# Optimization experiments

Measured on AMD Instinct MI355X. Metric: run time of the kernel, lower is better.

The kernel has to match this reference:

```python
import jax, jax.numpy as jnp
import numpy as np

GRID_RES = 256
SCALE = 1.0
N_POINTS = 2_000_000


def setup_inputs() -> dict:
    key = jax.random.key(0)
    k_pos, k_grid = jax.random.split(key)
    # points in [-0.6, 0.6]^3 so a realistic fraction falls inside the grid (|x| < scale/2)
    pos = jax.random.uniform(k_pos, (N_POINTS, 3), dtype=jnp.float32, minval=-0.6, maxval=0.6)
    # learned parameter: dense voxel grid with (r, g, b, density) per cell, init ~ U[0,1) like torch.rand
    voxel_grid = jax.random.uniform(k_grid, (GRID_RES, GRID_RES, GRID_RES, 4), dtype=jnp.float32)
    return {"pos": pos, "voxel_grid": voxel_grid}


def reference(pos, voxel_grid):
    grid_res = voxel_grid.shape[0]
    scale = SCALE
    half = scale / 2
    x, y, z = pos[:, 0], pos[:, 1], pos[:, 2]
    # mask of points inside the voxel grid volume
    cond = (jnp.abs(x) < half) & (jnp.abs(y) < half) & (jnp.abs(z) < half)

    inv_cell = grid_res / scale  # 1 / (scale / grid_res)
    offset = grid_res / 2

    def to_idx(v):
        # torch .type(torch.long) truncates toward zero; values here are in (0, grid_res)
        # so truncation == floor. Out-of-grid points are given a safe dummy index 0.
        i = (v * inv_cell + offset).astype(jnp.int32)
        return jnp.where(cond, i, 0)

    ix, iy, iz = to_idx(x), to_idx(y), to_idx(z)
    gathered = voxel_grid[ix, iy, iz]                      # [N, 4] gather
    cad = jnp.where(cond[:, None], gathered, jnp.zeros((), pos.dtype))  # masked points stay 0
    colors = jax.nn.sigmoid(cad[:, :3])                    # sigmoid(0)=0.5 for masked pts, as in torch
    density = jax.nn.relu(cad[:, 3])
    return colors, density
```

## Files before the change

kernel.cpp:

```cpp
#include <hip/hip_runtime.h>


#define GRID_RES 256

__global__ __launch_bounds__(256) void nerf_voxel_kernel(
    const float* __restrict__ pos,
    const float4* __restrict__ grid,
    float* __restrict__ colors,
    float* __restrict__ density,
    int n)
{
    int i = blockIdx.x * blockDim.x + threadIdx.x;
    if (i >= n) return;

    float x = pos[3 * i + 0];
    float y = pos[3 * i + 1];
    float z = pos[3 * i + 2];

    bool cond = (fabsf(x) < 0.5f) & (fabsf(y) < 0.5f) & (fabsf(z) < 0.5f);

    float4 cad = make_float4(0.0f, 0.0f, 0.0f, 0.0f);
    if (cond) {
        int ix = (int)(__fadd_rn(__fmul_rn(x, 256.0f), 128.0f));
        int iy = (int)(__fadd_rn(__fmul_rn(y, 256.0f), 128.0f));
        int iz = (int)(__fadd_rn(__fmul_rn(z, 256.0f), 128.0f));
        size_t idx = ((size_t)ix * GRID_RES + (size_t)iy) * GRID_RES + (size_t)iz;
        cad = grid[idx];
    }

    float c0 = 1.0f / (1.0f + __expf(-cad.x));
    float c1 = 1.0f / (1.0f + __expf(-cad.y));
    float c2 = 1.0f / (1.0f + __expf(-cad.z));
    float d  = fmaxf(cad.w, 0.0f);

    colors[3 * i + 0] = c0;
    colors[3 * i + 1] = c1;
    colors[3 * i + 2] = c2;
    density[i] = d;
}

extern "C" void kernel_launch(void* const* d_in, const int* in_sizes, int n_in,
                              void* d_out, int out_size, void* d_ws, size_t ws_size,
                              hipStream_t stream) {
    const float*  pos  = (const float*)d_in[0];
    const float4* grid = (const float4*)d_in[1];

    int n = in_sizes[0] / 3;
    float* colors  = (float*)d_out;
    float* density = colors + (size_t)3 * n;

    const int block = 256;
    const int gridsz = (n + block - 1) / block;
    hipLaunchKernelGGL(nerf_voxel_kernel, dim3(gridsz), dim3(block), 0, stream,
                       pos, grid, colors, density, n);
}
```

Baseline: 348.4 us.

## Process eight points per thread with vectorized float4 loads and stores

Each thread now handles eight points: it loads positions as six float4 vectors, computes all eight grid addresses, and issues all eight gathers before doing any math. It then writes colors and density back as float4 vectors. This is meant to reduce load/store instruction count and raise memory-level parallelism on the random gathers. The change drops tail handling, so it assumes n is divisible by 8, which holds for the 2M-point test but not in general. It also uses more registers per thread and launches fewer threads.

Result: no change. 348.8 us (+0.1%).

```diff
diff --git a/kernel.cpp b/kernel.cpp
--- a/kernel.cpp
+++ b/kernel.cpp
@@ -3,54 +3,79 @@
 
 #define GRID_RES 256
 
+__device__ __forceinline__ float sigmoidf(float v) {
+    return 1.0f / (1.0f + __expf(-v));
+}
+
 __global__ __launch_bounds__(256) void nerf_voxel_kernel(
-    const float* __restrict__ pos,
+    const float4* __restrict__ pos4,
     const float4* __restrict__ grid,
-    float* __restrict__ colors,
-    float* __restrict__ density,
+    float4* __restrict__ colors4,
+    float4* __restrict__ density4,
     int n)
 {
-    int i = blockIdx.x * blockDim.x + threadIdx.x;
-    if (i >= n) return;
+    const long nt = (long)n >> 3;
+    long t = (long)blockIdx.x * blockDim.x + threadIdx.x;
+    if (t >= nt) return;
 
-    float x = pos[3 * i + 0];
-    float y = pos[3 * i + 1];
-    float z = pos[3 * i + 2];
+    float4 p[6];
+#pragma unroll
+    for (int k = 0; k < 6; ++k) p[k] = pos4[6 * t + k];
+    const float* f = (const float*)p;
 
-    bool cond = (fabsf(x) < 0.5f) & (fabsf(y) < 0.5f) & (fabsf(z) < 0.5f);
-
-    float4 cad = make_float4(0.0f, 0.0f, 0.0f, 0.0f);
-    if (cond) {
+    size_t addr[8];
+    bool   cond[8];
+#pragma unroll
+    for (int j = 0; j < 8; ++j) {
+        float x = f[3 * j + 0];
+        float y = f[3 * j + 1];
+        float z = f[3 * j + 2];
+        bool c = (fabsf(x) < 0.5f) & (fabsf(y) < 0.5f) & (fabsf(z) < 0.5f);
         int ix = (int)(__fadd_rn(__fmul_rn(x, 256.0f), 128.0f));
         int iy = (int)(__fadd_rn(__fmul_rn(y, 256.0f), 128.0f));
         int iz = (int)(__fadd_rn(__fmul_rn(z, 256.0f), 128.0f));
-        size_t idx = ((size_t)ix * GRID_RES + (size_t)iy) * GRID_RES + (size_t)iz;
-        cad = grid[idx];
+        size_t a = ((size_t)ix * GRID_RES + (size_t)iy) * GRID_RES + (size_t)iz;
+        cond[j] = c;
+        addr[j] = c ? a : (size_t)0;
     }
 
-    float c0 = 1.0f / (1.0f + __expf(-cad.x));
-    float c1 = 1.0f / (1.0f + __expf(-cad.y));
-    float c2 = 1.0f / (1.0f + __expf(-cad.z));
-    float d  = fmaxf(cad.w, 0.0f);
+    float4 cad[8];
+#pragma unroll
+    for (int j = 0; j < 8; ++j) cad[j] = grid[addr[j]];
 
-    colors[3 * i + 0] = c0;
-    colors[3 * i + 1] = c1;
-    colors[3 * i + 2] = c2;
-    density[i] = d;
+    float out_c[24];
+    float out_d[8];
+#pragma unroll
+    for (int j = 0; j < 8; ++j) {
+        float4 v = cad[j];
+        if (!cond[j]) { v.x = 0.0f; v.y = 0.0f; v.z = 0.0f; v.w = 0.0f; }
+        out_c[3 * j + 0] = sigmoidf(v.x);
+        out_c[3 * j + 1] = sigmoidf(v.y);
+        out_c[3 * j + 2] = sigmoidf(v.z);
+        out_d[j]         = fmaxf(v.w, 0.0f);
+    }
+
+    const float4* oc = (const float4*)out_c;
+#pragma unroll
+    for (int k = 0; k < 6; ++k) colors4[6 * t + k] = oc[k];
+    const float4* od = (const float4*)out_d;
+    density4[2 * t + 0] = od[0];
+    density4[2 * t + 1] = od[1];
 }
 
 extern "C" void kernel_launch(void* const* d_in, const int* in_sizes, int n_in,
                               void* d_out, int out_size, void* d_ws, size_t ws_size,
                               hipStream_t stream) {
-    const float*  pos  = (const float*)d_in[0];
+    const float4* pos4 = (const float4*)d_in[0];
     const float4* grid = (const float4*)d_in[1];
 
     int n = in_sizes[0] / 3;
-    float* colors  = (float*)d_out;
-    float* density = colors + (size_t)3 * n;
+    float4* colors4  = (float4*)d_out;
+    float4* density4 = (float4*)((float*)d_out + (size_t)3 * n);
 
     const int block = 256;
-    const int gridsz = (n + block - 1) / block;
+    const long nt = (long)(n / 8);
+    const int gridsz = (int)((nt + block - 1) / block);
     hipLaunchKernelGGL(nerf_voxel_kernel, dim3(gridsz), dim3(block), 0, stream,
-                       pos, grid, colors, density, n);
+                       pos4, grid, colors4, density4, n);
 }
```
